# Performance work log

Measured on AMD Instinct MI355X. Metric: run time of the kernel, lower is better.

## Reference

```python
import jax, jax.numpy as jnp
import numpy as np
import math

H, KV, D, HID, WIN = 8, 4, 256, 2048, 1024  # heads, kv heads, head_dim, hidden, sliding window
B, S = 1, 2048

def _rms(x, scale):
    # Gemma3RMSNorm: hardcoded 1e-6 eps, (1+scale) gain
    var = jnp.mean(jnp.square(x), axis=-1, keepdims=True)
    return x * jax.lax.rsqrt(var + 1e-6) * (1.0 + scale)

def _rot_half(x):
    x1, x2 = jnp.split(x, 2, axis=-1)
    return jnp.concatenate((-x2, x1), axis=-1)

def setup_inputs() -> dict:
    key = jax.random.key(0)
    ks = jax.random.split(key, 8)
    x = jax.random.normal(ks[0], (B, S, HID), jnp.float32)
    attn_mask = jnp.ones((B, S), jnp.bool_)
    segment_pos = jnp.broadcast_to(jnp.arange(S, dtype=jnp.int32)[None], (B, S))
    # true RoPE tables, theta=1e6 (Gemma3 global layers)
    inv_freq = 1.0 / (1e6 ** (np.arange(0, D, 2, dtype=np.float32) / D))
    ang = np.arange(S, dtype=np.float32)[:, None] * inv_freq[None, :]  # [S, D/2]
    emb = np.concatenate([ang, ang], axis=-1)                          # [S, D]
    cos = jnp.asarray(np.cos(emb), jnp.float32)[None]                  # [1, S, D]
    sin = jnp.asarray(np.sin(emb), jnp.float32)[None]
    sd = 1.0 / math.sqrt(HID)
    wq = jax.random.normal(ks[1], (HID, H * D), jnp.float32) * sd
    wk = jax.random.normal(ks[2], (HID, KV * D), jnp.float32) * sd
    wv = jax.random.normal(ks[3], (HID, KV * D), jnp.float32) * sd
    wo = jax.random.normal(ks[4], (H * D, HID), jnp.float32) * (1.0 / math.sqrt(H * D))
    q_scale = jnp.zeros((D,), jnp.float32)  # zeros_init as in module
    k_scale = jnp.zeros((D,), jnp.float32)
    return dict(x=x, attn_mask=attn_mask, segment_pos=segment_pos, cos=cos, sin=sin,
                wq=wq, wk=wk, wv=wv, wo=wo, q_scale=q_scale, k_scale=k_scale)

def reference(x, attn_mask, segment_pos, cos, sin, wq, wk, wv, wo, q_scale, k_scale):
    b, s, _ = x.shape
    # projections -> [b, h, s, d]
    q = (x @ wq).reshape(b, s, H, D).transpose(0, 2, 1, 3)
    k = (x @ wk).reshape(b, s, KV, D).transpose(0, 2, 1, 3)
    v = (x @ wv).reshape(b, s, KV, D).transpose(0, 2, 1, 3)
    # per-head QK RMSNorm
    q = _rms(q, q_scale)
    k = _rms(k, k_scale)
    # RoPE (cos/sin broadcast over head axis, unsqueeze_dim=1)
    c, sn = cos[:, None], sin[:, None]
    q = q * c + _rot_half(q) * sn
    k = k * c + _rot_half(k) * sn
    # GQA: repeat-interleave kv heads
    rep = H // KV
    k = jnp.repeat(k, rep, axis=1)
    v = jnp.repeat(v, rep, axis=1)
    scores = jnp.einsum('bhqd,bhkd->bhqk', q, k) / math.sqrt(D)
    # causal + padding mask (q_len > 1 path, no image bidirectional mask)
    causal = jnp.tril(jnp.ones((s, s), jnp.bool_))
    mask = causal[None] & attn_mask[:, None, :]          # [b, q, kv]
    # sliding window mask (prefill: cache positions = arange)
    kvpos = jnp.arange(s)
    pos = segment_pos[:, :, None]
    sliding = (kvpos[None, None] > pos - WIN) & (kvpos[None, None] < pos + WIN)
    full = mask & sliding
    scores = scores + jnp.where(full[:, None], 0.0, -1e37)
    w = jax.nn.softmax(scores.astype(jnp.float32), axis=-1).astype(scores.dtype)
    out = jnp.einsum('bhqk,bhkd->bhqd', w, v)
    out = out.transpose(0, 2, 1, 3).reshape(b, s, H * D)
    return out @ wo
```

## Files before the change

kernel.cpp:

```cpp
#include <hip/hip_runtime.h>
#include <hip/hip_bf16.h>

#define S_LEN 2048
#define HID 2048
#define NH 8
#define NKV 4
#define HD 256
#define WIN 1024

typedef __hip_bfloat16 bf16;
typedef __attribute__((ext_vector_type(8))) short bf16x8;
typedef __attribute__((ext_vector_type(4))) float f32x4;

__device__ __forceinline__ void gld_lds16(void* lds, const void* g) {
    __builtin_amdgcn_global_load_lds(
        (const __attribute__((address_space(1))) unsigned int*)g,
        (__attribute__((address_space(3))) unsigned int*)lds,
        16, 0, 0);
}


__device__ __forceinline__ void transT_body(const float* __restrict__ src, bf16* __restrict__ dst,
                                            int R, int C, int r0, int c0) {
    __shared__ bf16 Ts[64][72];
    const int tid = threadIdx.x;
    {
        const int r = tid >> 2;
        const int cq = (tid & 3) * 16;
#pragma unroll
        for (int j = 0; j < 16; j += 4) {
            float4 v = *(const float4*)&src[(size_t)(r0 + r) * C + c0 + cq + j];
            Ts[cq + j + 0][r] = __float2bfloat16(v.x);
            Ts[cq + j + 1][r] = __float2bfloat16(v.y);
            Ts[cq + j + 2][r] = __float2bfloat16(v.z);
            Ts[cq + j + 3][r] = __float2bfloat16(v.w);
        }
    }
    __syncthreads();
    {
        const int c = tid >> 2;
        const int rq = (tid & 3) * 16;
#pragma unroll
        for (int j = 0; j < 16; j += 8)
            *(uint4*)&dst[(size_t)(c0 + c) * R + r0 + rq + j] = *(const uint4*)&Ts[c][rq + j];
    }
}

__global__ __launch_bounds__(256)
void prep_all(const float* __restrict__ xf, const float* __restrict__ wqf,
              const float* __restrict__ wkf, const float* __restrict__ wvf,
              const float* __restrict__ wof,
              bf16* __restrict__ xb, bf16* __restrict__ wqkvt, bf16* __restrict__ wot) {
    const int bid = blockIdx.x;
    if (bid < 2048) {
        const int i = bid * 256 + threadIdx.x;
        float4 a = ((const float4*)xf)[i * 2];
        float4 b = ((const float4*)xf)[i * 2 + 1];
        union { uint4 v; bf16 h[8]; } u;
        u.h[0] = __float2bfloat16(a.x); u.h[1] = __float2bfloat16(a.y);
        u.h[2] = __float2bfloat16(a.z); u.h[3] = __float2bfloat16(a.w);
        u.h[4] = __float2bfloat16(b.x); u.h[5] = __float2bfloat16(b.y);
        u.h[6] = __float2bfloat16(b.z); u.h[7] = __float2bfloat16(b.w);
        ((uint4*)xb)[i] = u.v;
    } else if (bid < 4096) {
        const int t = bid - 2048;
        const int bx = t & 63, by = t >> 6;
        const float* src; int C, c0, drow0;
        if (bx < 32)      { src = wqf; C = 2048; c0 = bx * 64;        drow0 = bx * 64; }
        else if (bx < 48) { src = wkf; C = 1024; c0 = (bx - 32) * 64; drow0 = 2048 + (bx - 32) * 64; }
        else              { src = wvf; C = 1024; c0 = (bx - 48) * 64; drow0 = 3072 + (bx - 48) * 64; }
        bf16* dshift = wqkvt + ((size_t)drow0 - c0) * HID;
        transT_body(src, dshift, HID, C, by * 64, c0);
    } else {
        const int t = bid - 4096;
        const int bx = t & 31, by = t >> 5;
        transT_body(wof, wot, NH * HD, HID, by * 64, bx * 64);
    }
}

template<int MODE>
__global__ __launch_bounds__(512, 2)
void gemm8p(const bf16* __restrict__ A, const bf16* __restrict__ Bt,
            bf16* __restrict__ Cb,
            bf16* __restrict__ Qo, bf16* __restrict__ Ko, bf16* __restrict__ Vto) {
    extern __shared__ bf16 smem[];
    bf16* AsP = smem;
    bf16* BsP = smem + 3 * 256 * 64;

    const int tid = threadIdx.x;
    const int w = tid >> 6, lane = tid & 63;
    const int lnm = lane & 15, quad = lane >> 4;
    const int wr = w >> 1, wc = w & 1;
    const int r8 = lane >> 3;
    const int swz = ((lane & 7) ^ r8) * 8;

    const int bid = blockIdx.x;
    const int xcd = bid & 7, idx = bid >> 3;
    int m0, n0, kbeg, nt;
    size_t zoff = 0;
    if constexpr (MODE == 1) {
        const int m_t = (xcd >> 2) * 4 + (idx >> 3);
        const int n_t = (xcd & 3) * 8 + (idx & 7);
        m0 = m_t * 256; n0 = n_t * 128; kbeg = 0; nt = 2048 / 64;
    } else {
        const int z   = xcd >> 2;
        const int n_t = (xcd & 3) * 4 + (idx & 3);
        const int m_t = idx >> 2;
        m0 = m_t * 256; n0 = n_t * 128; kbeg = z * 1024; nt = 1024 / 64;
        zoff = (size_t)z * 2048 * 2048;
    }
    const int K = 2048;

    const bf16* pA[4];
#pragma unroll
    for (int g = 0; g < 4; ++g)
        pA[g] = A + (size_t)(m0 + w * 32 + g * 8 + r8) * K + kbeg + swz;
    const bf16* pB[2];
#pragma unroll
    for (int g = 0; g < 2; ++g)
        pB[g] = Bt + (size_t)(n0 + w * 16 + g * 8 + r8) * K + kbeg + swz;
    const int dA = w * 32 * 64;
    const int dB = w * 16 * 64;

#define STG_A(slot, g, t) gld_lds16(AsP + (slot) * 16384 + dA + (g) * 512, pA[g] + (t) * 64)
#define STG_B(slot, g, t) gld_lds16(BsP + (slot) * 8192  + dB + (g) * 512, pB[g] + (t) * 64)
#define LDFRAG(base, row, kh) \
    (*(const bf16x8*)((base) + (row) * 64 + (((((kh) << 2) | quad) ^ ((row) & 7)) << 3)))

    f32x4 acc[4][4];
#pragma unroll
    for (int i = 0; i < 4; ++i)
#pragma unroll
        for (int j = 0; j < 4; ++j) acc[i][j] = (f32x4){0.f, 0.f, 0.f, 0.f};

    STG_A(0, 0, 0); STG_A(0, 1, 0); STG_A(0, 2, 0); STG_A(0, 3, 0);
    STG_B(0, 0, 0); STG_B(0, 1, 0);
    STG_A(1, 0, 1); STG_A(1, 1, 1); STG_A(1, 2, 1); STG_A(1, 3, 1);
    STG_B(1, 0, 1); STG_B(1, 1, 1);
    asm volatile("s_waitcnt vmcnt(6)" ::: "memory");
    __builtin_amdgcn_sched_barrier(0);
    __builtin_amdgcn_s_barrier();

    int sc = 0;
    for (int t = 0; t < nt; ++t) {
        const int ss = (sc == 0) ? 2 : sc - 1;
        const bf16* As_ = AsP + sc * 16384;
        const bf16* Bs_ = BsP + sc * 8192;
        const bool pf = (t + 2 < nt);

        bf16x8 a0[2][2], b[4][2];
#pragma unroll
        for (int tm = 0; tm < 2; ++tm)
#pragma unroll
            for (int kh = 0; kh < 2; ++kh)
                a0[tm][kh] = LDFRAG(As_, wr * 64 + tm * 16 + lnm, kh);
#pragma unroll
        for (int tn = 0; tn < 4; ++tn)
#pragma unroll
            for (int kh = 0; kh < 2; ++kh)
                b[tn][kh] = LDFRAG(Bs_, wc * 64 + tn * 16 + lnm, kh);
        if (pf) { STG_A(ss, 0, t + 2); STG_A(ss, 1, t + 2); STG_B(ss, 0, t + 2); }
        __builtin_amdgcn_s_barrier();
        asm volatile("s_waitcnt lgkmcnt(0)" ::: "memory");
        __builtin_amdgcn_sched_barrier(0);
        __builtin_amdgcn_s_setprio(1);
#pragma unroll
        for (int kh = 0; kh < 2; ++kh)
#pragma unroll
            for (int tm = 0; tm < 2; ++tm)
#pragma unroll
                for (int tn = 0; tn < 4; ++tn)
                    acc[tm][tn] = __builtin_amdgcn_mfma_f32_16x16x32_bf16(
                        a0[tm][kh], b[tn][kh], acc[tm][tn], 0, 0, 0);
        __builtin_amdgcn_s_setprio(0);
        __builtin_amdgcn_s_barrier();

        bf16x8 a1[2][2];
#pragma unroll
        for (int tm = 0; tm < 2; ++tm)
#pragma unroll
            for (int kh = 0; kh < 2; ++kh)
                a1[tm][kh] = LDFRAG(As_, wr * 64 + (tm + 2) * 16 + lnm, kh);
        if (pf) { STG_A(ss, 2, t + 2); STG_A(ss, 3, t + 2); STG_B(ss, 1, t + 2); }
        if (pf) { asm volatile("s_waitcnt vmcnt(6)" ::: "memory"); }
        else    { asm volatile("s_waitcnt vmcnt(0)" ::: "memory"); }
        __builtin_amdgcn_sched_barrier(0);
        __builtin_amdgcn_s_barrier();
        asm volatile("s_waitcnt lgkmcnt(0)" ::: "memory");
        __builtin_amdgcn_sched_barrier(0);
        __builtin_amdgcn_s_setprio(1);
#pragma unroll
        for (int kh = 0; kh < 2; ++kh)
#pragma unroll
            for (int tm = 0; tm < 2; ++tm)
#pragma unroll
                for (int tn = 0; tn < 4; ++tn)
                    acc[tm + 2][tn] = __builtin_amdgcn_mfma_f32_16x16x32_bf16(
                        a1[tm][kh], b[tn][kh], acc[tm + 2][tn], 0, 0, 0);
        __builtin_amdgcn_s_setprio(0);
        __builtin_amdgcn_s_barrier();

        sc = (sc == 2) ? 0 : sc + 1;
    }
#undef STG_A
#undef STG_B
#undef LDFRAG

#pragma unroll
    for (int tm = 0; tm < 4; ++tm)
#pragma unroll
        for (int tn = 0; tn < 4; ++tn)
#pragma unroll
            for (int r = 0; r < 4; ++r) {
                const int row = m0 + wr * 64 + tm * 16 + quad * 4 + r;
                const int col = n0 + wc * 64 + tn * 16 + lnm;
                const float v = acc[tm][tn][r];
                if constexpr (MODE == 2) {
                    Cb[zoff + (size_t)row * 2048 + col] = __float2bfloat16(v);
                } else {
                    if (col < 2048)
                        Qo[(size_t)row * (NH * HD) + col] = __float2bfloat16(v);
                    else if (col < 3072)
                        Ko[(size_t)row * (NKV * HD) + col - 2048] = __float2bfloat16(v);
                    else
                        Vto[(size_t)(col - 3072) * S_LEN + row] = __float2bfloat16(v);
                }
            }
}

__global__ __launch_bounds__(256)
void splitk_add(const bf16* __restrict__ p, float* __restrict__ out) {
    const int i = blockIdx.x * 256 + threadIdx.x;
    union { uint4 v; bf16 h[8]; } a, b;
    a.v = ((const uint4*)p)[i];
    b.v = ((const uint4*)(p + (size_t)2048 * 2048))[i];
    float4 o0, o1;
    o0.x = (float)a.h[0] + (float)b.h[0]; o0.y = (float)a.h[1] + (float)b.h[1];
    o0.z = (float)a.h[2] + (float)b.h[2]; o0.w = (float)a.h[3] + (float)b.h[3];
    o1.x = (float)a.h[4] + (float)b.h[4]; o1.y = (float)a.h[5] + (float)b.h[5];
    o1.z = (float)a.h[6] + (float)b.h[6]; o1.w = (float)a.h[7] + (float)b.h[7];
    ((float4*)out)[i * 2]     = o0;
    ((float4*)out)[i * 2 + 1] = o1;
}

__global__ __launch_bounds__(256)
void rmsrope_kernel(bf16* __restrict__ Q, bf16* __restrict__ Kb,
                    const float* __restrict__ cosb, const float* __restrict__ sinb,
                    const float* __restrict__ qscale, const float* __restrict__ kscale,
                    float qmul) {
    __shared__ float cf[256], sf[256], qsl[256], ksl[256];
    const int p = blockIdx.x;
    const int tid = threadIdx.x, w = tid >> 6, lane = tid & 63;

    cf[tid]  = cosb[(size_t)p * HD + tid];
    sf[tid]  = sinb[(size_t)p * HD + tid];
    qsl[tid] = qscale[tid];
    ksl[tid] = kscale[tid];
    __syncthreads();

    const int d0 = lane * 2;
    const float c0 = cf[d0],       c1 = cf[d0 + 1];
    const float cA = cf[d0 + 128], cB = cf[d0 + 129];
    const float s0 = sf[d0],       s1 = sf[d0 + 1];
    const float sA = sf[d0 + 128], sB = sf[d0 + 129];

#pragma unroll
    for (int i = 0; i < 3; ++i) {
        const int hg = w + i * 4;
        bf16* base;
        const float* scl;
        float mul;
        if (hg < NH) { base = Q + (size_t)p * (NH * HD) + hg * HD; scl = qsl; mul = qmul; }
        else         { base = Kb + (size_t)p * (NKV * HD) + (hg - NH) * HD; scl = ksl; mul = 1.f; }

        float x0 = (float)base[d0],       x1 = (float)base[d0 + 1];
        float y0 = (float)base[d0 + 128], y1 = (float)base[d0 + 129];

        float ss = x0 * x0 + x1 * x1 + y0 * y0 + y1 * y1;
#pragma unroll
        for (int off = 32; off > 0; off >>= 1) ss += __shfl_xor(ss, off, 64);
        const float r = rsqrtf(ss * (1.0f / (float)HD) + 1e-6f);

        x0 *= r * (1.f + scl[d0]);
        x1 *= r * (1.f + scl[d0 + 1]);
        y0 *= r * (1.f + scl[d0 + 128]);
        y1 *= r * (1.f + scl[d0 + 129]);

        base[d0]       = __float2bfloat16((x0 * c0 - y0 * s0) * mul);
        base[d0 + 1]   = __float2bfloat16((x1 * c1 - y1 * s1) * mul);
        base[d0 + 128] = __float2bfloat16((y0 * cA + x0 * sA) * mul);
        base[d0 + 129] = __float2bfloat16((y1 * cB + x1 * sB) * mul);
    }
}

#define NCHUNK 4

__device__ __forceinline__ unsigned pkbf(float a, float b) {
    union { bf16 h; unsigned short u; } ca, cb;
    ca.h = __float2bfloat16(a); cb.h = __float2bfloat16(b);
    return (unsigned)ca.u | ((unsigned)cb.u << 16);
}

__global__ __launch_bounds__(512)
void attn_mfma(const bf16* __restrict__ Q, const bf16* __restrict__ K,
               const bf16* __restrict__ Vt, bf16* __restrict__ Op,
               float2* __restrict__ ml) {
    extern __shared__ bf16 smem[];
    bf16* KsP = smem;
    bf16* VsP = smem + 2 * 32 * 256;
    const int qt = blockIdx.x, h = blockIdx.y, chunk = blockIdx.z, kvh = h >> 1;
    const int tid = threadIdx.x, w = tid >> 6, lane = tid & 63;
    const int lnm = lane & 15, quad = lane >> 4;

    bf16x8 qf[8];
    const int qrow = qt * 128 + w * 16 + lnm;
#pragma unroll
    for (int s = 0; s < 8; ++s)
        qf[s] = *(const bf16x8*)&Q[(size_t)qrow * HID + h * HD + s * 32 + quad * 8];

    f32x4 o[16];
#pragma unroll
    for (int i = 0; i < 16; ++i) o[i] = (f32x4){0.f, 0.f, 0.f, 0.f};
    float M = -3e38f, L = 0.f;

    const int ktlo = (qt >= 8) ? (4 * qt - 32) : 0;
    const int kthi = 4 * qt + 3;
    const int ntile = kthi - ktlo + 1;
    const int c0 = ktlo + (chunk * ntile) / NCHUNK;
    const int c1 = ktlo + ((chunk + 1) * ntile) / NCHUNK - 1;

    const int srow = w * 4 + (lane >> 5);
    const int sunit = lane & 31;
    const bf16* kg = K + (size_t)kvh * HD;
    const int vrow = lane >> 2;
    const int vgu  = (lane & 3) ^ ((lane >> 3) & 3);
    const bf16* vsrc = Vt + ((size_t)(kvh * HD + w * 32 + vrow)) * S_LEN + vgu * 8;

#define STAGE_K(kt_, buf_)                                                        \
    {                                                                             \
        _Pragma("unroll")                                                         \
        for (int cc = 0; cc < 2; ++cc) {                                          \
            const int r_ = srow + cc * 2;                                         \
            const int ug_ = sunit ^ (r_ & 7);                                     \
            gld_lds16(KsP + (buf_) * 8192 + (w * 4 + cc * 2) * 256,               \
                      kg + (size_t)((kt_) * 32 + r_) * (NKV * HD) + ug_ * 8);     \
        }                                                                         \
    }
#define STAGE_V(kt_, vb_)                                                         \
    {                                                                             \
        _Pragma("unroll")                                                         \
        for (int cc = 0; cc < 2; ++cc)                                            \
            gld_lds16(VsP + (vb_) * 8192 + (w * 32 + cc * 16) * 32,               \
                      vsrc + (size_t)cc * 16 * S_LEN + (kt_) * 32);               \
    }
#define KFRAG(buf_, t_, s_) \
    (*(const bf16x8*)&KsP[(buf_) * 8192 + ((t_) * 16 + lnm) * 256 + ((((s_) * 4 + quad) ^ (lnm & 7)) * 8)])
#define VFRAG(vb_, t2_) \
    (*(const bf16x8*)&VsP[(vb_) * 8192 + ((t2_) * 16 + lnm) * 32 + ((quad ^ ((lnm >> 1) & 3)) * 8)])

    if (c0 <= c1) {
        STAGE_K(c0, 0);

        for (int kt = c0; kt <= c1; ++kt) {
            const int buf = (kt - c0) & 1;
            STAGE_V(kt, buf);
            if (kt < c1) STAGE_K(kt + 1, buf ^ 1);
            if (kt < c1) { asm volatile("s_waitcnt vmcnt(4)" ::: "memory"); }
            else         { asm volatile("s_waitcnt vmcnt(2)" ::: "memory"); }
            __builtin_amdgcn_sched_barrier(0);
            __builtin_amdgcn_s_barrier();

            f32x4 s4[2];
            s4[0] = (f32x4){0.f, 0.f, 0.f, 0.f};
            s4[1] = (f32x4){0.f, 0.f, 0.f, 0.f};
            __builtin_amdgcn_s_setprio(1);
#pragma unroll
            for (int t = 0; t < 2; ++t)
#pragma unroll
                for (int s = 0; s < 8; ++s)
                    s4[t] = __builtin_amdgcn_mfma_f32_16x16x32_bf16(
                        KFRAG(buf, t, s), qf[s], s4[t], 0, 0, 0);
            __builtin_amdgcn_s_setprio(0);

#pragma unroll
            for (int t = 0; t < 2; ++t)
#pragma unroll
                for (int r = 0; r < 4; ++r) {
                    const int n_g = kt * 32 + t * 16 + quad * 4 + r;
                    if (n_g > qrow || n_g + (WIN - 1) < qrow) s4[t][r] = -1e30f;
                }

            float mx = fmaxf(fmaxf(fmaxf(s4[0][0], s4[0][1]), fmaxf(s4[0][2], s4[0][3])),
                             fmaxf(fmaxf(s4[1][0], s4[1][1]), fmaxf(s4[1][2], s4[1][3])));
            mx = fmaxf(mx, __shfl_xor(mx, 16, 64));
            mx = fmaxf(mx, __shfl_xor(mx, 32, 64));

            if (!__all(mx <= M + 8.f)) {
                const float Mn = fmaxf(M, mx);
                const float al = __expf(M - Mn);
                M = Mn;
                L *= al;
                float alr[4];
#pragma unroll
                for (int r = 0; r < 4; ++r) alr[r] = __shfl(al, quad * 4 + r, 64);
#pragma unroll
                for (int t2 = 0; t2 < 16; ++t2)
#pragma unroll
                    for (int r = 0; r < 4; ++r) o[t2][r] *= alr[r];
            }

            float rs = 0.f;
            unsigned u00, u01, u10, u11;
            {
                float p0 = __expf(s4[0][0] - M), p1 = __expf(s4[0][1] - M);
                float p2 = __expf(s4[0][2] - M), p3 = __expf(s4[0][3] - M);
                rs += (p0 + p1) + (p2 + p3);
                u00 = pkbf(p0, p1); u01 = pkbf(p2, p3);
                p0 = __expf(s4[1][0] - M); p1 = __expf(s4[1][1] - M);
                p2 = __expf(s4[1][2] - M); p3 = __expf(s4[1][3] - M);
                rs += (p0 + p1) + (p2 + p3);
                u10 = pkbf(p0, p1); u11 = pkbf(p2, p3);
            }
            rs += __shfl_xor(rs, 16, 64);
            rs += __shfl_xor(rs, 32, 64);
            L += rs;

            const int slo = lnm + 16 * (2 * (quad & 1));
            const int shi = slo + 16;
            const int A0 = __shfl((int)u00, slo, 64), A1 = __shfl((int)u01, slo, 64);
            const int A2 = __shfl((int)u00, shi, 64), A3 = __shfl((int)u01, shi, 64);
            const int B0 = __shfl((int)u10, slo, 64), B1 = __shfl((int)u11, slo, 64);
            const int B2 = __shfl((int)u10, shi, 64), B3 = __shfl((int)u11, shi, 64);
            union { bf16x8 v; int i4[4]; } pa;
            pa.i4[0] = (quad < 2) ? A0 : B0;
            pa.i4[1] = (quad < 2) ? A1 : B1;
            pa.i4[2] = (quad < 2) ? A2 : B2;
            pa.i4[3] = (quad < 2) ? A3 : B3;

            if (kt < c1) { asm volatile("s_waitcnt vmcnt(2)" ::: "memory"); }
            else         { asm volatile("s_waitcnt vmcnt(0)" ::: "memory"); }
            __builtin_amdgcn_sched_barrier(0);
            __builtin_amdgcn_s_barrier();

            __builtin_amdgcn_s_setprio(1);
#pragma unroll
            for (int t2 = 0; t2 < 16; ++t2)
                o[t2] = __builtin_amdgcn_mfma_f32_16x16x32_bf16(pa.v, VFRAG(buf, t2), o[t2], 0, 0, 0);
            __builtin_amdgcn_s_setprio(0);
        }
    }
#undef STAGE_K
#undef STAGE_V
#undef KFRAG
#undef VFRAG

    const float rL = (L > 0.f) ? (1.f / L) : 0.f;
    float rr[4];
#pragma unroll
    for (int r = 0; r < 4; ++r) rr[r] = __shfl(rL, quad * 4 + r, 64);
    bf16* Opc = Op + (size_t)chunk * S_LEN * HID;
#pragma unroll
    for (int t2 = 0; t2 < 16; ++t2)
#pragma unroll
        for (int r = 0; r < 4; ++r)
            Opc[(size_t)(qt * 128 + w * 16 + quad * 4 + r) * HID + h * HD + t2 * 16 + lnm] =
                __float2bfloat16(o[t2][r] * rr[r]);
    if (quad == 0)
        ml[((size_t)chunk * S_LEN + qt * 128 + w * 16 + lnm) * NH + h] = make_float2(M, L);
}

__global__ __launch_bounds__(256)
void attn_combine(const bf16* __restrict__ Op, const float2* __restrict__ ml,
                  bf16* __restrict__ O) {
    const int row = blockIdx.x, t = threadIdx.x;
    const int h = t >> 5;
    float2 c[NCHUNK];
    float Mx = -3e38f;
#pragma unroll
    for (int i = 0; i < NCHUNK; ++i) {
        c[i] = ml[((size_t)i * S_LEN + row) * NH + h];
        Mx = fmaxf(Mx, c[i].x);
    }
    float wsum = 0.f, wgt[NCHUNK];
#pragma unroll
    for (int i = 0; i < NCHUNK; ++i) {
        wgt[i] = c[i].y * __expf(c[i].x - Mx);
        wsum += wgt[i];
    }
    const float inv = 1.0f / wsum;
    const size_t base = (size_t)row * HID + t * 8;
    float acc[8] = {0.f, 0.f, 0.f, 0.f, 0.f, 0.f, 0.f, 0.f};
#pragma unroll
    for (int i = 0; i < NCHUNK; ++i) {
        union { uint4 v; bf16 h8[8]; } a;
        a.v = *(const uint4*)(Op + (size_t)i * S_LEN * HID + base);
#pragma unroll
        for (int j = 0; j < 8; ++j) acc[j] += wgt[i] * (float)a.h8[j];
    }
    union { uint4 v; bf16 h8[8]; } ou;
#pragma unroll
    for (int j = 0; j < 8; ++j) ou.h8[j] = __float2bfloat16(acc[j] * inv);
    *(uint4*)(O + base) = ou.v;
}

extern "C" void kernel_launch(void* const* d_in, const int* in_sizes, int n_in,
                              void* d_out, int out_size, void* d_ws, size_t ws_size,
                              hipStream_t stream) {
    const float* xf   = (const float*)d_in[0];
    const float* cosb = (const float*)d_in[3];
    const float* sinb = (const float*)d_in[4];
    const float* wqf  = (const float*)d_in[5];
    const float* wkf  = (const float*)d_in[6];
    const float* wvf  = (const float*)d_in[7];
    const float* wof  = (const float*)d_in[8];
    const float* qs   = (const float*)d_in[9];
    const float* ks   = (const float*)d_in[10];
    float* out = (float*)d_out;
    char* ws = (char*)d_ws;

    bf16*   wot   = (bf16*)(ws);
    bf16*   Qb    = (bf16*)(ws + ( 8ull << 20));
    bf16*   Kb    = (bf16*)(ws + (16ull << 20));
    bf16*   Vtb   = (bf16*)(ws + (20ull << 20));
    bf16*   wqkvt = (bf16*)(ws + (24ull << 20));
    bf16*   xb    = (bf16*)(ws + (40ull << 20));
    bf16*   Op    = (bf16*)(ws + (24ull << 20));
    bf16*   Ab    = (bf16*)(ws + (40ull << 20));
    bf16*   pk    = (bf16*)(ws + (24ull << 20));
    float2* ml    = (float2*)(ws + (56ull << 20));

    dim3 blk(256);

    static bool attr_done = false;
    if (!attr_done) {
        (void)hipFuncSetAttribute(reinterpret_cast<const void*>(gemm8p<1>),
                                  hipFuncAttributeMaxDynamicSharedMemorySize, 147456);
        (void)hipFuncSetAttribute(reinterpret_cast<const void*>(gemm8p<2>),
                                  hipFuncAttributeMaxDynamicSharedMemorySize, 147456);
        (void)hipFuncSetAttribute(reinterpret_cast<const void*>(attn_mfma),
                                  hipFuncAttributeMaxDynamicSharedMemorySize, 65536);
        attr_done = true;
    }

    prep_all<<<5120, blk, 0, stream>>>(xf, wqf, wkf, wvf, wof, xb, wqkvt, wot);

    gemm8p<1><<<dim3(256), dim3(512), 147456, stream>>>(
        xb, wqkvt, nullptr, Qb, Kb, Vtb);

    rmsrope_kernel<<<dim3(S_LEN), blk, 0, stream>>>(
        Qb, Kb, cosb, sinb, qs, ks, 0.0625f);

    attn_mfma<<<dim3(S_LEN / 128, NH, NCHUNK), dim3(512), 65536, stream>>>(
        Qb, Kb, Vtb, Op, ml);
    attn_combine<<<dim3(S_LEN), blk, 0, stream>>>(Op, ml, Ab);

    gemm8p<2><<<dim3(256), dim3(512), 147456, stream>>>(
        Ab, wot, pk, nullptr, nullptr, nullptr);
    splitk_add<<<2048, blk, 0, stream>>>(pk, out);
}
```

Before: 255.3 us.

## Switch attention kernel to 32x32x16 MFMA with 4 waves of 32 query rows

Rewrites the attention inner loop to use 32x32x16 bf16 MFMA instead of 16x16x32. Each of 4 waves (256 threads, down from 512) now owns 32 query rows, and the K/V LDS staging swizzles and fragment layouts are redone to match. The aim is to halve the per-wave LDS fragment traffic per FLOP and to simplify the P-matrix shuffle to a single xor-32 exchange. In exchange, register pressure rises (16 Q fragments, 128 accumulator floats per lane), and having fewer waves per block may reduce latency hiding. It also drops the c0<=c1 guard.

```diff
diff --git a/kernel.cpp b/kernel.cpp
--- a/kernel.cpp
+++ b/kernel.cpp
@@ -11,6 +11,7 @@
 typedef __hip_bfloat16 bf16;
 typedef __attribute__((ext_vector_type(8))) short bf16x8;
 typedef __attribute__((ext_vector_type(4))) float f32x4;
+typedef __attribute__((ext_vector_type(16))) float f32x16;
 
 __device__ __forceinline__ void gld_lds16(void* lds, const void* g) {
     __builtin_amdgcn_global_load_lds(
@@ -301,7 +302,7 @@
     return (unsigned)ca.u | ((unsigned)cb.u << 16);
 }
 
-__global__ __launch_bounds__(512)
+__global__ __launch_bounds__(256)
 void attn_mfma(const bf16* __restrict__ Q, const bf16* __restrict__ K,
                const bf16* __restrict__ Vt, bf16* __restrict__ Op,
                float2* __restrict__ ml) {
@@ -310,17 +311,19 @@
     bf16* VsP = smem + 2 * 32 * 256;
     const int qt = blockIdx.x, h = blockIdx.y, chunk = blockIdx.z, kvh = h >> 1;
     const int tid = threadIdx.x, w = tid >> 6, lane = tid & 63;
-    const int lnm = lane & 15, quad = lane >> 4;
-
-    bf16x8 qf[8];
-    const int qrow = qt * 128 + w * 16 + lnm;
-#pragma unroll
-    for (int s = 0; s < 8; ++s)
-        qf[s] = *(const bf16x8*)&Q[(size_t)qrow * HID + h * HD + s * 32 + quad * 8];
-
-    f32x4 o[16];
-#pragma unroll
-    for (int i = 0; i < 16; ++i) o[i] = (f32x4){0.f, 0.f, 0.f, 0.f};
+    const int l31 = lane & 31, hi = lane >> 5;
+
+    bf16x8 qf[16];
+    const int qrow = qt * 128 + w * 32 + l31;
+#pragma unroll
+    for (int s = 0; s < 16; ++s)
+        qf[s] = *(const bf16x8*)&Q[(size_t)qrow * HID + h * HD + s * 16 + hi * 8];
+
+    f32x16 o[8];
+#pragma unroll
+    for (int i = 0; i < 8; ++i)
+#pragma unroll
+        for (int r = 0; r < 16; ++r) o[i][r] = 0.f;
     float M = -3e38f, L = 0.f;
 
     const int ktlo = (qt >= 8) ? (4 * qt - 32) : 0;
@@ -329,70 +332,66 @@
     const int c0 = ktlo + (chunk * ntile) / NCHUNK;
     const int c1 = ktlo + ((chunk + 1) * ntile) / NCHUNK - 1;
 
-    const int srow = w * 4 + (lane >> 5);
-    const int sunit = lane & 31;
     const bf16* kg = K + (size_t)kvh * HD;
-    const int vrow = lane >> 2;
-    const int vgu  = (lane & 3) ^ ((lane >> 3) & 3);
-    const bf16* vsrc = Vt + ((size_t)(kvh * HD + w * 32 + vrow)) * S_LEN + vgu * 8;
-
-#define STAGE_K(kt_, buf_)                                                        \
-    {                                                                             \
-        _Pragma("unroll")                                                         \
-        for (int cc = 0; cc < 2; ++cc) {                                          \
-            const int r_ = srow + cc * 2;                                         \
-            const int ug_ = sunit ^ (r_ & 7);                                     \
-            gld_lds16(KsP + (buf_) * 8192 + (w * 4 + cc * 2) * 256,               \
-                      kg + (size_t)((kt_) * 32 + r_) * (NKV * HD) + ug_ * 8);     \
-        }                                                                         \
-    }
-#define STAGE_V(kt_, vb_)                                                         \
-    {                                                                             \
-        _Pragma("unroll")                                                         \
-        for (int cc = 0; cc < 2; ++cc)                                            \
-            gld_lds16(VsP + (vb_) * 8192 + (w * 32 + cc * 16) * 32,               \
-                      vsrc + (size_t)cc * 16 * S_LEN + (kt_) * 32);               \
-    }
-#define KFRAG(buf_, t_, s_) \
-    (*(const bf16x8*)&KsP[(buf_) * 8192 + ((t_) * 16 + lnm) * 256 + ((((s_) * 4 + quad) ^ (lnm & 7)) * 8)])
-#define VFRAG(vb_, t2_) \
-    (*(const bf16x8*)&VsP[(vb_) * 8192 + ((t2_) * 16 + lnm) * 32 + ((quad ^ ((lnm >> 1) & 3)) * 8)])
-
-    if (c0 <= c1) {
+    const bf16* vg = Vt + (size_t)(kvh * HD) * S_LEN;
+
+#define STAGE_K(kt_, buf_)                                                          \
+    {                                                                               \
+        _Pragma("unroll")                                                           \
+        for (int cc = 0; cc < 4; ++cc) {                                            \
+            const int gu_ = (lane & 31) ^ (cc * 2) ^ hi ^ w;                        \
+            gld_lds16(KsP + (buf_) * 8192 + (w * 8 + cc * 2) * 256,                 \
+                      kg + (size_t)((kt_) * 32 + w * 8 + cc * 2 + hi) * (NKV * HD)  \
+                         + gu_ * 8);                                                \
+        }                                                                           \
+    }
+#define STAGE_V(kt_, vb_)                                                           \
+    {                                                                               \
+        _Pragma("unroll")                                                           \
+        for (int cc = 0; cc < 4; ++cc) {                                            \
+            const int gv_ = (lane & 3) ^ ((lane >> 3) & 3) ^ ((cc * 2 + hi) & 3);   \
+            gld_lds16(VsP + (vb_) * 8192 + (w * 64 + cc * 16) * 32,                 \
+                      vg + (size_t)(w * 64 + cc * 16 + (lane >> 2)) * S_LEN         \
+                         + (kt_) * 32 + gv_ * 8);                                   \
+        }                                                                           \
+    }
+#define KFRAG(buf_, s_) \
+    (*(const bf16x8*)&KsP[(buf_) * 8192 + l31 * 256 + \
+        (((2 * (s_) + hi) ^ (lane & 7) ^ ((lane >> 3) & 3)) * 8)])
+#define VFRAG(vb_, dblk_, ks_) \
+    (*(const bf16x8*)&VsP[(vb_) * 8192 + ((dblk_) * 32 + l31) * 32 + \
+        (((2 * (ks_) + hi) ^ ((lane >> 1) & 3) ^ ((lane >> 3) & 3)) * 8)])
+
+    {
         STAGE_K(c0, 0);
 
         for (int kt = c0; kt <= c1; ++kt) {
             const int buf = (kt - c0) & 1;
             STAGE_V(kt, buf);
             if (kt < c1) STAGE_K(kt + 1, buf ^ 1);
-            if (kt < c1) { asm volatile("s_waitcnt vmcnt(4)" ::: "memory"); }
-            else         { asm volatile("s_waitcnt vmcnt(2)" ::: "memory"); }
+            if (kt < c1) { asm volatile("s_waitcnt vmcnt(8)" ::: "memory"); }
+            else         { asm volatile("s_waitcnt vmcnt(4)" ::: "memory"); }
             __builtin_amdgcn_sched_barrier(0);
             __builtin_amdgcn_s_barrier();
 
-            f32x4 s4[2];
-            s4[0] = (f32x4){0.f, 0.f, 0.f, 0.f};
-            s4[1] = (f32x4){0.f, 0.f, 0.f, 0.f};
+            f32x16 sv;
+#pragma unroll
+            for (int r = 0; r < 16; ++r) sv[r] = 0.f;
             __builtin_amdgcn_s_setprio(1);
 #pragma unroll
-            for (int t = 0; t < 2; ++t)
-#pragma unroll
-                for (int s = 0; s < 8; ++s)
-                    s4[t] = __builtin_amdgcn_mfma_f32_16x16x32_bf16(
-                        KFRAG(buf, t, s), qf[s], s4[t], 0, 0, 0);
+            for (int s = 0; s < 16; ++s)
+                sv = __builtin_amdgcn_mfma_f32_32x32x16_bf16(KFRAG(buf, s), qf[s], sv, 0, 0, 0);
             __builtin_amdgcn_s_setprio(0);
 
 #pragma unroll
-            for (int t = 0; t < 2; ++t)
-#pragma unroll
-                for (int r = 0; r < 4; ++r) {
-                    const int n_g = kt * 32 + t * 16 + quad * 4 + r;
-                    if (n_g > qrow || n_g + (WIN - 1) < qrow) s4[t][r] = -1e30f;
-                }
-
-            float mx = fmaxf(fmaxf(fmaxf(s4[0][0], s4[0][1]), fmaxf(s4[0][2], s4[0][3])),
-                             fmaxf(fmaxf(s4[1][0], s4[1][1]), fmaxf(s4[1][2], s4[1][3])));
-            mx = fmaxf(mx, __shfl_xor(mx, 16, 64));
+            for (int r = 0; r < 16; ++r) {
+                const int n_g = kt * 32 + (r & 3) + 8 * (r >> 2) + 4 * hi;
+                if (n_g > qrow || n_g + (WIN - 1) < qrow) sv[r] = -1e30f;
+            }
+
+            float mx = sv[0];
+#pragma unroll
+            for (int r = 1; r < 16; ++r) mx = fmaxf(mx, sv[r]);
             mx = fmaxf(mx, __shfl_xor(mx, 32, 64));
 
             if (!__all(mx <= M + 8.f)) {
@@ -400,52 +399,53 @@
                 const float al = __expf(M - Mn);
                 M = Mn;
                 L *= al;
-                float alr[4];
-#pragma unroll
-                for (int r = 0; r < 4; ++r) alr[r] = __shfl(al, quad * 4 + r, 64);
-#pragma unroll
-                for (int t2 = 0; t2 < 16; ++t2)
-#pragma unroll
-                    for (int r = 0; r < 4; ++r) o[t2][r] *= alr[r];
+                float alr[16];
+#pragma unroll
+                for (int r = 0; r < 16; ++r)
+                    alr[r] = __shfl(al, (r & 3) + 8 * (r >> 2) + 4 * hi, 64);
+#pragma unroll
+                for (int i = 0; i < 8; ++i)
+#pragma unroll
+                    for (int r = 0; r < 16; ++r) o[i][r] *= alr[r];
             }
 
             float rs = 0.f;
-            unsigned u00, u01, u10, u11;
-            {
-                float p0 = __expf(s4[0][0] - M), p1 = __expf(s4[0][1] - M);
-                float p2 = __expf(s4[0][2] - M), p3 = __expf(s4[0][3] - M);
-                rs += (p0 + p1) + (p2 + p3);
-                u00 = pkbf(p0, p1); u01 = pkbf(p2, p3);
-                p0 = __expf(s4[1][0] - M); p1 = __expf(s4[1][1] - M);
-                p2 = __expf(s4[1][2] - M); p3 = __expf(s4[1][3] - M);
-                rs += (p0 + p1) + (p2 + p3);
-                u10 = pkbf(p0, p1); u11 = pkbf(p2, p3);
+            unsigned u[8];
+#pragma unroll
+            for (int i = 0; i < 8; ++i) {
+                const float p0 = __expf(sv[2 * i] - M), p1 = __expf(sv[2 * i + 1] - M);
+                rs += p0 + p1;
+                u[i] = pkbf(p0, p1);
             }
-            rs += __shfl_xor(rs, 16, 64);
             rs += __shfl_xor(rs, 32, 64);
             L += rs;
 
-            const int slo = lnm + 16 * (2 * (quad & 1));
-            const int shi = slo + 16;
-            const int A0 = __shfl((int)u00, slo, 64), A1 = __shfl((int)u01, slo, 64);
-            const int A2 = __shfl((int)u00, shi, 64), A3 = __shfl((int)u01, shi, 64);
-            const int B0 = __shfl((int)u10, slo, 64), B1 = __shfl((int)u11, slo, 64);
-            const int B2 = __shfl((int)u10, shi, 64), B3 = __shfl((int)u11, shi, 64);
-            union { bf16x8 v; int i4[4]; } pa;
-            pa.i4[0] = (quad < 2) ? A0 : B0;
-            pa.i4[1] = (quad < 2) ? A1 : B1;
-            pa.i4[2] = (quad < 2) ? A2 : B2;
-            pa.i4[3] = (quad < 2) ? A3 : B3;
-
-            if (kt < c1) { asm volatile("s_waitcnt vmcnt(2)" ::: "memory"); }
+            unsigned pu[8];
+#pragma unroll
+            for (int i = 0; i < 8; ++i) pu[i] = (unsigned)__shfl_xor((int)u[i], 32, 64);
+            union { bf16x8 v; unsigned i4[4]; } pa0, pa1;
+            if (hi == 0) {
+                pa0.i4[0] = u[0]; pa0.i4[1] = u[1]; pa0.i4[2] = pu[0]; pa0.i4[3] = pu[1];
+                pa1.i4[0] = u[4]; pa1.i4[1] = u[5]; pa1.i4[2] = pu[4]; pa1.i4[3] = pu[5];
+            } else {
+                pa0.i4[0] = pu[2]; pa0.i4[1] = pu[3]; pa0.i4[2] = u[2]; pa0.i4[3] = u[3];
+                pa1.i4[0] = pu[6]; pa1.i4[1] = pu[7]; pa1.i4[2] = u[6]; pa1.i4[3] = u[7];
+            }
+
+            if (kt < c1) { asm volatile("s_waitcnt vmcnt(4)" ::: "memory"); }
             else         { asm volatile("s_waitcnt vmcnt(0)" ::: "memory"); }
             __builtin_amdgcn_sched_barrier(0);
             __builtin_amdgcn_s_barrier();
 
             __builtin_amdgcn_s_setprio(1);
 #pragma unroll
-            for (int t2 = 0; t2 < 16; ++t2)
-                o[t2] = __builtin_amdgcn_mfma_f32_16x16x32_bf16(pa.v, VFRAG(buf, t2), o[t2], 0, 0, 0);
+            for (int dblk = 0; dblk < 8; ++dblk)
+                o[dblk] = __builtin_amdgcn_mfma_f32_32x32x16_bf16(
+                    pa0.v, VFRAG(buf, dblk, 0), o[dblk], 0, 0, 0);
+#pragma unroll
+            for (int dblk = 0; dblk < 8; ++dblk)
+                o[dblk] = __builtin_amdgcn_mfma_f32_32x32x16_bf16(
+                    pa1.v, VFRAG(buf, dblk, 1), o[dblk], 0, 0, 0);
             __builtin_amdgcn_s_setprio(0);
         }
     }
@@ -455,18 +455,19 @@
 #undef VFRAG
 
     const float rL = (L > 0.f) ? (1.f / L) : 0.f;
-    float rr[4];
-#pragma unroll
-    for (int r = 0; r < 4; ++r) rr[r] = __shfl(rL, quad * 4 + r, 64);
+    float rr[16];
+#pragma unroll
+    for (int r = 0; r < 16; ++r)
+        rr[r] = __shfl(rL, (r & 3) + 8 * (r >> 2) + 4 * hi, 64);
     bf16* Opc = Op + (size_t)chunk * S_LEN * HID;
 #pragma unroll
-    for (int t2 = 0; t2 < 16; ++t2)
-#pragma unroll
-        for (int r = 0; r < 4; ++r)
-            Opc[(size_t)(qt * 128 + w * 16 + quad * 4 + r) * HID + h * HD + t2 * 16 + lnm] =
-                __float2bfloat16(o[t2][r] * rr[r]);
-    if (quad == 0)
-        ml[((size_t)chunk * S_LEN + qt * 128 + w * 16 + lnm) * NH + h] = make_float2(M, L);
+    for (int dblk = 0; dblk < 8; ++dblk)
+#pragma unroll
+        for (int r = 0; r < 16; ++r)
+            Opc[(size_t)(qt * 128 + w * 32 + (r & 3) + 8 * (r >> 2) + 4 * hi) * HID
+                + h * HD + dblk * 32 + l31] = __float2bfloat16(o[dblk][r] * rr[r]);
+    if (lane < 32)
+        ml[((size_t)chunk * S_LEN + qt * 128 + w * 32 + lane) * NH + h] = make_float2(M, L);
 }
 
 __global__ __launch_bounds__(256)
@@ -550,7 +551,7 @@
     rmsrope_kernel<<<dim3(S_LEN), blk, 0, stream>>>(
         Qb, Kb, cosb, sinb, qs, ks, 0.0625f);
 
-    attn_mfma<<<dim3(S_LEN / 128, NH, NCHUNK), dim3(512), 65536, stream>>>(
+    attn_mfma<<<dim3(S_LEN / 128, NH, NCHUNK), blk, 65536, stream>>>(
         Qb, Kb, Vtb, Op, ml);
     attn_combine<<<dim3(S_LEN), blk, 0, stream>>>(Op, ml, Ab);
 
```

Result: slower. 265.2 us (+3.9%).
